# Kernel tuning notes

Measured on AMD Instinct MI355X. Metric: run time of the kernel, lower is better.

Reference implementation:

```python
import jax, jax.numpy as jnp
import numpy as np

B, S, D, H = 2, 2048, 1024, 16
HD = D // H  # head dim = 64

def setup_inputs() -> dict:
    key = jax.random.key(0)
    ks = jax.random.split(key, 11)
    s = 0.02
    return {
        "query": jax.random.normal(ks[0], (B, S, D), jnp.float32),
        "key_in": jax.random.normal(ks[1], (B, S, D), jnp.float32),
        "value": jax.random.normal(ks[2], (B, S, D), jnp.float32),
        "Wq": jax.random.normal(ks[3], (D, D), jnp.float32) * s,
        "bq": jnp.zeros((D,), jnp.float32),
        "Wk": jax.random.normal(ks[4], (D, D), jnp.float32) * s,
        "bk": jnp.zeros((D,), jnp.float32),
        "Wv": jax.random.normal(ks[5], (D, D), jnp.float32) * s,
        "bv": jnp.zeros((D,), jnp.float32),
        "Wo": jax.random.normal(ks[6], (D, D), jnp.float32) * s,
        "bo": jnp.zeros((D,), jnp.float32),
    }

def _split_heads(x):
    b, s, _ = x.shape
    return x.reshape(b, s, H, HD).transpose(0, 2, 1, 3)  # [B,H,S,HD]

def reference(query, key_in, value, Wq, bq, Wk, bk, Wv, bv, Wo, bo):
    q = _split_heads(query @ Wq + bq)
    k = _split_heads(key_in @ Wk + bk)
    v = _split_heads(value @ Wv + bv)
    scores = jnp.einsum("bhqd,bhkd->bhqk", q, k) / jnp.sqrt(jnp.float32(HD))
    weights = jax.nn.softmax(scores, axis=-1)  # dropout = identity (eval)
    ctx = jnp.einsum("bhqk,bhkd->bhqd", weights, v)
    ctx = ctx.transpose(0, 2, 1, 3).reshape(query.shape[0], -1, D)
    return ctx @ Wo + bo
```

## Files before the change

kernel.cpp:

```cpp
#include <hip/hip_runtime.h>
#include <hip/hip_bf16.h>


typedef __attribute__((ext_vector_type(8))) short short8;
typedef __attribute__((ext_vector_type(4))) short short4v;
typedef __attribute__((ext_vector_type(4))) float f32x4;

static __device__ __forceinline__ short f2bf(float f) {
    union { float f; unsigned u; } c; c.f = f;
    unsigned r = c.u + 0x7fff + ((c.u >> 16) & 1);
    return (short)(r >> 16);
}

static __device__ __forceinline__ unsigned pk_bf16(float a, float b) {
    union { __hip_bfloat162 h; unsigned u; } c;
    c.h = __float22bfloat162_rn(make_float2(a, b));
    return c.u;
}

typedef const void __attribute__((address_space(1)))* gas_ptr;
typedef void __attribute__((address_space(3)))* las_ptr;
static __device__ __forceinline__ void gload16(const void* g, void* l) {
    __builtin_amdgcn_global_load_lds((gas_ptr)g, (las_ptr)l, 16, 0, 0);
}

__global__ __launch_bounds__(256) void prep(
    const float* __restrict__ X0, const float* __restrict__ X1,
    const float* __restrict__ X2, short* __restrict__ Abf,
    const float* __restrict__ W0, const float* __restrict__ W1,
    const float* __restrict__ W2, const float* __restrict__ W3,
    short* __restrict__ Wt)
{
    __shared__ float tile[32][33];
    const int bid = blockIdx.x;
    if (bid < 6144) {
        const int zz = bid >> 11, xb = bid & 2047;
        const float* X = zz == 0 ? X0 : zz == 1 ? X1 : X2;
        short* o = Abf + ((size_t)zz << 22);
        const int i = (xb * 256 + threadIdx.x) * 8;
        const float4 a = *(const float4*)(X + i);
        const float4 b = *(const float4*)(X + i + 4);
        uint4 r;
        r.x = pk_bf16(a.x, a.y); r.y = pk_bf16(a.z, a.w);
        r.z = pk_bf16(b.x, b.y); r.w = pk_bf16(b.z, b.w);
        *(uint4*)(o + i) = r;
    } else {
        const int wid = bid - 6144;
        const int z = wid >> 10;
        const float* W = z == 0 ? W0 : z == 1 ? W1 : z == 2 ? W2 : W3;
        short* O = Wt + ((size_t)z << 20);
        const int k0 = (wid & 31) * 32, n0 = ((wid >> 5) & 31) * 32;
        const int tx = threadIdx.x & 31, ty = threadIdx.x >> 5;
        #pragma unroll
        for (int j = 0; j < 32; j += 8)
            tile[ty + j][tx] = W[(k0 + ty + j) * 1024 + n0 + tx];
        __syncthreads();
        #pragma unroll
        for (int j = 0; j < 32; j += 8)
            O[(n0 + ty + j) * 1024 + k0 + tx] = f2bf(tile[tx][ty + j]);
    }
}

#define GEMM_CORE(Aa, Ba)                                                     \
    __shared__ short Al[2][2048];                           \
    __shared__ short Bl[2][4096];                          \
    const int t = threadIdx.x;                                                \
    const int m0 = blockIdx.y * 64, n0 = blockIdx.x * 128;                    \
    const int lane = t & 63, w = t >> 6;                                      \
    const int lm = lane & 15, lg = lane >> 4;                                 \
    const int wr = w >> 1, wc = w & 1;                                        \
    f32x4 acc[2][4] = {};                                                     \
    STAGE(0, 0);                                                              \
    __syncthreads();                                                          \
    int buf = 0;                                                              \
    for (int kk = 0; kk < 32; ++kk) {                                         \
        if (kk < 31) STAGE(buf ^ 1, (kk + 1) * 32);                           \
        const short* Ab = Al[buf];                                            \
        const short* Bb = Bl[buf];                                            \
        short8 af[2], bfr[4];                                                 \
        _Pragma("unroll")                                                     \
        for (int mf = 0; mf < 2; ++mf)                                        \
            af[mf] = *(const short8*)(Ab + (wr * 32 + mf * 16 + lm) * 32 + lg * 8); \
        _Pragma("unroll")                                                     \
        for (int nf = 0; nf < 4; ++nf)                                        \
            bfr[nf] = *(const short8*)(Bb + (wc * 64 + nf * 16 + lm) * 32 + lg * 8); \
        _Pragma("unroll")                                                     \
        for (int mf = 0; mf < 2; ++mf)                                        \
            _Pragma("unroll")                                                 \
            for (int nf = 0; nf < 4; ++nf)                                    \
                acc[mf][nf] = __builtin_amdgcn_mfma_f32_16x16x32_bf16(        \
                    af[mf], bfr[nf], acc[mf][nf], 0, 0, 0);                   \
        __syncthreads();                                                      \
        buf ^= 1;                                                             \
    }

#define STAGE(buf, k0) do {                                                   \
    gload16(Aa + (size_t)(m0 + (t >> 2)) * 1024 + (k0) + (t & 3) * 8,         \
            &Al[buf][w * 512]);                                               \
    _Pragma("unroll")                                                         \
    for (int j = 0; j < 2; ++j) {                                             \
        const int c = j * 256 + t;                                            \
        gload16(Ba + (size_t)(n0 + (c >> 2)) * 1024 + (k0) + (c & 3) * 8,     \
                &Bl[buf][j * 2048 + w * 512]);                                \
    }                                                                         \
} while (0)

__global__ __launch_bounds__(256) void gemmqkv(
    const short* __restrict__ Abase, const short* __restrict__ Wt,
    const float* __restrict__ bq, const float* __restrict__ bk,
    const float* __restrict__ bv, short* __restrict__ Qh,
    short* __restrict__ Kh, short* __restrict__ Vt, float qscale)
{
    const int z = blockIdx.z;
    const short* Aa = Abase + ((size_t)z << 22);
    const short* Ba = Wt + ((size_t)z << 20);
    const float* bias = z == 0 ? bq : z == 1 ? bk : bv;
    short* O = z == 0 ? Qh : z == 1 ? Kh : Vt;
    const float scale = z == 0 ? qscale : 1.0f;

    GEMM_CORE(Aa, Ba)

    #pragma unroll
    for (int mf = 0; mf < 2; ++mf) {
        const int mb = m0 + wr * 32 + mf * 16 + lg * 4;
        #pragma unroll
        for (int nf = 0; nf < 4; ++nf) {
            const int n = n0 + wc * 64 + nf * 16 + lm;
            const float bs = bias[n];
            if (z == 2) {
                short4v sv;
                #pragma unroll
                for (int i = 0; i < 4; ++i)
                    sv[i] = f2bf(acc[mf][nf][i] + bs);
                const int addr = (((mb >> 11) * 16 + (n >> 6)) * 64 + (n & 63)) * 2048 + (mb & 2047);
                *(short4v*)&O[addr] = sv;
            } else {
                #pragma unroll
                for (int i = 0; i < 4; ++i) {
                    const int m = mb + i;
                    const int addr = (((m >> 11) * 16 + (n >> 6)) * 2048 + (m & 2047)) * 64 + (n & 63);
                    O[addr] = f2bf(scale * (acc[mf][nf][i] + bs));
                }
            }
        }
    }
}

__global__ __launch_bounds__(256) void gemmo(
    const short* __restrict__ Aa, const short* __restrict__ Ba,
    const float* __restrict__ bias, float* __restrict__ Out)
{
    GEMM_CORE(Aa, Ba)

    #pragma unroll
    for (int mf = 0; mf < 2; ++mf) {
        const int mb = m0 + wr * 32 + mf * 16 + lg * 4;
        #pragma unroll
        for (int nf = 0; nf < 4; ++nf) {
            const int n = n0 + wc * 64 + nf * 16 + lm;
            const float bs = bias[n];
            #pragma unroll
            for (int i = 0; i < 4; ++i)
                Out[(mb + i) * 1024 + n] = acc[mf][nf][i] + bs;
        }
    }
}
#undef STAGE
#undef GEMM_CORE

__global__ __launch_bounds__(512, 4) void attn_k(
    const short* __restrict__ Q, const short* __restrict__ K,
    const short* __restrict__ V, short* __restrict__ Ctx)
{
    __shared__ short Kl[2][128][64];
    __shared__ short Vl[2][64][128];
    __shared__ short Pl[8][16][64];
    const int t = threadIdx.x;
    const int qt = blockIdx.x, bh = blockIdx.y;
    const int lane = t & 63, w = t >> 6;
    const int lm = lane & 15, lg = lane >> 4;
    const int swz = (lm & 7) << 3;
    const int swc = lm & 7;

    const int qrow = qt * 128 + w * 16 + lm;
    short8 qf[2];
    #pragma unroll
    for (int ks = 0; ks < 2; ++ks)
        qf[ks] = *(const short8*)(Q + ((size_t)bh * 2048 + qrow) * 64 + ks * 32 + lg * 8);

    float m_run = -3e38f, l_run = 0.f;
    f32x4 o_acc[4] = {};

    const int rk = t >> 2, ck = t & 3;
    const int rv = t >> 3, cv = t & 7;
    const short* Kg = K + ((size_t)bh * 2048 + rk) * 64 + ck * 16;
    const short* Vg = V + ((size_t)bh * 64 + rv) * 2048 + cv * 16;
    const int koff0 = rk * 64 + ((ck * 2) ^ (rk & 7)) * 8;
    const int koff1 = rk * 64 + ((ck * 2 + 1) ^ (rk & 7)) * 8;
    const int vc0 = cv * 2, vc1 = cv * 2 + 1;
    const int voff0 = rv * 128 + ((vc0 & 8) | ((vc0 & 7) ^ (rv & 7))) * 8;
    const int voff1 = rv * 128 + ((vc1 & 8) | ((vc1 & 7) ^ (rv & 7))) * 8;

    {
        short8 a = *(const short8*)(Kg);
        short8 b = *(const short8*)(Kg + 8);
        short8 c = *(const short8*)(Vg);
        short8 d = *(const short8*)(Vg + 8);
        *(short8*)((short*)Kl[0] + koff0) = a;
        *(short8*)((short*)Kl[0] + koff1) = b;
        *(short8*)((short*)Vl[0] + voff0) = c;
        *(short8*)((short*)Vl[0] + voff1) = d;
    }

    short* prow = &Pl[w][lm][0];
    int cur = 0;

    for (int kt = 0; kt < 16; ++kt) {
        __syncthreads();

        short8 kn0, kn1, vn0, vn1;
        const bool pfn = (kt < 15);
        if (pfn) {
            const short* Kgn = Kg + (size_t)(kt + 1) * 8192;
            const short* Vgn = Vg + (kt + 1) * 128;
            kn0 = *(const short8*)(Kgn);
            kn1 = *(const short8*)(Kgn + 8);
            vn0 = *(const short8*)(Vgn);
            vn1 = *(const short8*)(Vgn + 8);
        }

        const short* Kc = (const short*)Kl[cur];
        const short* Vc = (const short*)Vl[cur];

        #pragma unroll
        for (int h = 0; h < 2; ++h) {
            f32x4 sa[4] = {};
            #pragma unroll
            for (int nf = 0; nf < 4; ++nf) {
                const int rr = h * 64 + nf * 16 + lm;
                #pragma unroll
                for (int ks = 0; ks < 2; ++ks) {
                    const short8 kf = *(const short8*)(Kc + rr * 64 + ((ks * 4 + lg) ^ swc) * 8);
                    sa[nf] = __builtin_amdgcn_mfma_f32_16x16x32_bf16(kf, qf[ks], sa[nf], 0, 0, 0);
                }
            }

            float mt = sa[0][0];
            #pragma unroll
            for (int nf = 0; nf < 4; ++nf)
                #pragma unroll
                for (int i = 0; i < 4; ++i)
                    mt = fmaxf(mt, sa[nf][i]);
            mt = fmaxf(mt, __shfl_xor(mt, 16));
            mt = fmaxf(mt, __shfl_xor(mt, 32));
            if (__any(mt > m_run + 8.0f)) {
                const float mn = fmaxf(m_run, mt);
                const float alpha = exp2f(m_run - mn);
                l_run *= alpha;
                #pragma unroll
                for (int nf = 0; nf < 4; ++nf)
                    #pragma unroll
                    for (int i = 0; i < 4; ++i)
                        o_acc[nf][i] *= alpha;
                m_run = mn;
            }
            float rs = 0.f;
            #pragma unroll
            for (int nf = 0; nf < 4; ++nf)
                #pragma unroll
                for (int i = 0; i < 4; ++i) {
                    const float e = exp2f(sa[nf][i] - m_run);
                    sa[nf][i] = e;
                    rs += e;
                }
            rs += __shfl_xor(rs, 16);
            rs += __shfl_xor(rs, 32);
            l_run += rs;

            #pragma unroll
            for (int nf = 0; nf < 4; ++nf) {
                uint2 pv;
                pv.x = pk_bf16(sa[nf][0], sa[nf][1]);
                pv.y = pk_bf16(sa[nf][2], sa[nf][3]);
                *(uint2*)(prow + ((nf * 16 + lg * 4) ^ swz)) = pv;
            }
            short8 pf[2];
            #pragma unroll
            for (int ks = 0; ks < 2; ++ks)
                pf[ks] = *(const short8*)(prow + ((ks * 32 + lg * 8) ^ swz));

            if (h == 0 && pfn) {
                short* Kn = (short*)Kl[cur ^ 1];
                short* Vn = (short*)Vl[cur ^ 1];
                *(short8*)(Kn + koff0) = kn0;
                *(short8*)(Kn + koff1) = kn1;
                *(short8*)(Vn + voff0) = vn0;
                *(short8*)(Vn + voff1) = vn1;
            }

            #pragma unroll
            for (int nf = 0; nf < 4; ++nf) {
                const int rr = nf * 16 + lm;
                #pragma unroll
                for (int ks = 0; ks < 2; ++ks) {
                    const short8 vf = *(const short8*)(Vc + rr * 128 + (h * 8 + ((ks * 4 + lg) ^ swc)) * 8);
                    o_acc[nf] = __builtin_amdgcn_mfma_f32_16x16x32_bf16(vf, pf[ks], o_acc[nf], 0, 0, 0);
                }
            }
        }
        cur ^= 1;
    }

    const float inv = 1.f / l_run;
    const int b = bh >> 4, h = bh & 15;
    short* outp = Ctx + ((size_t)b * 2048 + qrow) * 1024 + h * 64 + lg * 4;
    #pragma unroll
    for (int nf = 0; nf < 4; ++nf) {
        uint2 pk;
        pk.x = pk_bf16(o_acc[nf][0] * inv, o_acc[nf][1] * inv);
        pk.y = pk_bf16(o_acc[nf][2] * inv, o_acc[nf][3] * inv);
        *(uint2*)(outp + nf * 16) = pk;
    }
}

extern "C" void kernel_launch(void* const* d_in, const int* in_sizes, int n_in,
                              void* d_out, int out_size, void* d_ws, size_t ws_size,
                              hipStream_t stream)
{
    const float* query  = (const float*)d_in[0];
    const float* key_in = (const float*)d_in[1];
    const float* value  = (const float*)d_in[2];
    const float* Wq = (const float*)d_in[3];
    const float* bq = (const float*)d_in[4];
    const float* Wk = (const float*)d_in[5];
    const float* bk = (const float*)d_in[6];
    const float* Wv = (const float*)d_in[7];
    const float* bv = (const float*)d_in[8];
    const float* Wo = (const float*)d_in[9];
    const float* bo = (const float*)d_in[10];
    float* out = (float*)d_out;

    char* ws = (char*)d_ws;
    short* Wt  = (short*)(ws);
    short* Abf = (short*)(ws + (8  << 20));
    short* Qh  = (short*)(ws + (32 << 20));
    short* Kh  = (short*)(ws + (40 << 20));
    short* Vt  = (short*)(ws + (48 << 20));
    short* Ctx = Abf;

    const float qscale = 0.125f * 1.44269504088896f;

    hipLaunchKernelGGL(prep, dim3(10240), dim3(256), 0, stream,
                       query, key_in, value, Abf, Wq, Wk, Wv, Wo, Wt);
    hipLaunchKernelGGL(gemmqkv, dim3(8, 64, 3), dim3(256), 0, stream,
                       Abf, Wt, bq, bk, bv, Qh, Kh, Vt, qscale);
    hipLaunchKernelGGL(attn_k, dim3(16, 32), dim3(512), 0, stream,
                       Qh, Kh, Vt, Ctx);
    hipLaunchKernelGGL(gemmo, dim3(8, 64), dim3(256), 0, stream,
                       Ctx, Wt + (3 << 20), bo, out);
}
```

Measured before the change: 163.1 us.

## Compute full 128-key score tile before one online-softmax update; split V LDS layout

The attention loop now computes S for both 64-key halves of the 128-key tile first, then runs one max reduction, one conditional rescale and one row-sum reduction over all 128 keys. This halves the per-tile softmax bookkeeping (shuffles, __any vote, possible o_acc rescale) and lets the QK MFMAs issue back to back. The V shared-memory tile is reorganized into two 64x64 halves with an 8-chunk XOR swizzle, so reads index a half by offset. The cost is more live accumulator registers (32 floats of scores), which may raise register pressure under the 512-thread, 4-block launch bound.

```diff
diff --git a/kernel.cpp b/kernel.cpp
--- a/kernel.cpp
+++ b/kernel.cpp
@@ -173,7 +173,7 @@
     const short* __restrict__ V, short* __restrict__ Ctx)
 {
     __shared__ short Kl[2][128][64];
-    __shared__ short Vl[2][64][128];
+    __shared__ short Vl[2][2][64][64];
     __shared__ short Pl[8][16][64];
     const int t = threadIdx.x;
     const int qt = blockIdx.x, bh = blockIdx.y;
@@ -197,9 +197,9 @@
     const short* Vg = V + ((size_t)bh * 64 + rv) * 2048 + cv * 16;
     const int koff0 = rk * 64 + ((ck * 2) ^ (rk & 7)) * 8;
     const int koff1 = rk * 64 + ((ck * 2 + 1) ^ (rk & 7)) * 8;
-    const int vc0 = cv * 2, vc1 = cv * 2 + 1;
-    const int voff0 = rv * 128 + ((vc0 & 8) | ((vc0 & 7) ^ (rv & 7))) * 8;
-    const int voff1 = rv * 128 + ((vc1 & 8) | ((vc1 & 7) ^ (rv & 7))) * 8;
+    const int vhalf = (cv >> 2) * 4096;
+    const int voff0 = vhalf + rv * 64 + (((cv * 2) & 7) ^ (rv & 7)) * 8;
+    const int voff1 = vhalf + rv * 64 + (((cv * 2 + 1) & 7) ^ (rv & 7)) * 8;
 
     {
         short8 a = *(const short8*)(Kg);
@@ -232,56 +232,62 @@
         const short* Kc = (const short*)Kl[cur];
         const short* Vc = (const short*)Vl[cur];
 
-        #pragma unroll
-        for (int h = 0; h < 2; ++h) {
-            f32x4 sa[4] = {};
+        f32x4 sa[2][4] = {};
+        #pragma unroll
+        for (int h = 0; h < 2; ++h)
             #pragma unroll
             for (int nf = 0; nf < 4; ++nf) {
                 const int rr = h * 64 + nf * 16 + lm;
                 #pragma unroll
                 for (int ks = 0; ks < 2; ++ks) {
                     const short8 kf = *(const short8*)(Kc + rr * 64 + ((ks * 4 + lg) ^ swc) * 8);
-                    sa[nf] = __builtin_amdgcn_mfma_f32_16x16x32_bf16(kf, qf[ks], sa[nf], 0, 0, 0);
+                    sa[h][nf] = __builtin_amdgcn_mfma_f32_16x16x32_bf16(kf, qf[ks], sa[h][nf], 0, 0, 0);
                 }
             }
 
-            float mt = sa[0][0];
+        float mt = sa[0][0][0];
+        #pragma unroll
+        for (int h = 0; h < 2; ++h)
             #pragma unroll
             for (int nf = 0; nf < 4; ++nf)
                 #pragma unroll
                 for (int i = 0; i < 4; ++i)
-                    mt = fmaxf(mt, sa[nf][i]);
-            mt = fmaxf(mt, __shfl_xor(mt, 16));
-            mt = fmaxf(mt, __shfl_xor(mt, 32));
-            if (__any(mt > m_run + 8.0f)) {
-                const float mn = fmaxf(m_run, mt);
-                const float alpha = exp2f(m_run - mn);
-                l_run *= alpha;
-                #pragma unroll
-                for (int nf = 0; nf < 4; ++nf)
-                    #pragma unroll
-                    for (int i = 0; i < 4; ++i)
-                        o_acc[nf][i] *= alpha;
-                m_run = mn;
-            }
-            float rs = 0.f;
+                    mt = fmaxf(mt, sa[h][nf][i]);
+        mt = fmaxf(mt, __shfl_xor(mt, 16));
+        mt = fmaxf(mt, __shfl_xor(mt, 32));
+        if (__any(mt > m_run + 8.0f)) {
+            const float mn = fmaxf(m_run, mt);
+            const float alpha = exp2f(m_run - mn);
+            l_run *= alpha;
             #pragma unroll
             for (int nf = 0; nf < 4; ++nf)
                 #pragma unroll
+                for (int i = 0; i < 4; ++i)
+                    o_acc[nf][i] *= alpha;
+            m_run = mn;
+        }
+        float rs = 0.f;
+        #pragma unroll
+        for (int h = 0; h < 2; ++h)
+            #pragma unroll
+            for (int nf = 0; nf < 4; ++nf)
+                #pragma unroll
                 for (int i = 0; i < 4; ++i) {
-                    const float e = exp2f(sa[nf][i] - m_run);
-                    sa[nf][i] = e;
+                    const float e = exp2f(sa[h][nf][i] - m_run);
+                    sa[h][nf][i] = e;
                     rs += e;
                 }
-            rs += __shfl_xor(rs, 16);
-            rs += __shfl_xor(rs, 32);
-            l_run += rs;
-
+        rs += __shfl_xor(rs, 16);
+        rs += __shfl_xor(rs, 32);
+        l_run += rs;
+
+        #pragma unroll
+        for (int h = 0; h < 2; ++h) {
             #pragma unroll
             for (int nf = 0; nf < 4; ++nf) {
                 uint2 pv;
-                pv.x = pk_bf16(sa[nf][0], sa[nf][1]);
-                pv.y = pk_bf16(sa[nf][2], sa[nf][3]);
+                pv.x = pk_bf16(sa[h][nf][0], sa[h][nf][1]);
+                pv.y = pk_bf16(sa[h][nf][2], sa[h][nf][3]);
                 *(uint2*)(prow + ((nf * 16 + lg * 4) ^ swz)) = pv;
             }
             short8 pf[2];
@@ -303,7 +309,7 @@
                 const int rr = nf * 16 + lm;
                 #pragma unroll
                 for (int ks = 0; ks < 2; ++ks) {
-                    const short8 vf = *(const short8*)(Vc + rr * 128 + (h * 8 + ((ks * 4 + lg) ^ swc)) * 8);
+                    const short8 vf = *(const short8*)(Vc + h * 4096 + rr * 64 + ((ks * 4 + lg) ^ swc) * 8);
                     o_acc[nf] = __builtin_amdgcn_mfma_f32_16x16x32_bf16(vf, pf[ks], o_acc[nf], 0, 0, 0);
                 }
             }
```

After: 161.3 us. No clear change (-1.1%).
